# Performance work log

Measured on AMD Instinct MI355X. Metric: run time of the kernel, lower is better.

## Reference

```python
import jax, jax.numpy as jnp
import numpy as np

B, P, D, H, A, C = 256, 512, 16, 256, 8, 2
HID = 256
IN_MLP = H + A + 1  # 265


def setup_inputs() -> dict:
    key = jax.random.key(0)
    ks = jax.random.split(key, 12)
    s = 0.05  # small init for recurrent stability
    return {
        "particles": jax.random.normal(ks[0], (B, P, D), jnp.float32),
        "weights": jax.random.uniform(ks[1], (B, P), jnp.float32),
        "actions": jax.random.normal(ks[2], (B, A), jnp.float32),
        "time": jax.random.uniform(ks[3], (B,), jnp.float32) * 100.0,
        "Wi": jax.random.normal(ks[4], (D + 1, 3 * H), jnp.float32) * s,
        "bi": jnp.zeros((3 * H,), jnp.float32),
        "Wh_rz": jax.random.normal(ks[5], (H, 2 * H), jnp.float32) * s,
        "Wh_n": jax.random.normal(ks[6], (H, H), jnp.float32) * s,
        "bn": jnp.zeros((H,), jnp.float32),
        "mlp_W1": jax.random.normal(ks[7], (C, IN_MLP, HID), jnp.float32) * s,
        "mlp_b1": jnp.zeros((C, HID), jnp.float32),
        "mlp_W2": jax.random.normal(ks[8], (C, HID, HID), jnp.float32) * s,
        "mlp_b2": jnp.zeros((C, HID), jnp.float32),
        "mlp_W3": jax.random.normal(ks[9], (C, HID, 1), jnp.float32) * s,
        "mlp_b3": jnp.zeros((C, 1), jnp.float32),
        "num_time_steps": 100,
    }


def reference(particles, weights, actions, time, Wi, bi, Wh_rz, Wh_n, bn,
              mlp_W1, mlp_b1, mlp_W2, mlp_b2, mlp_W3, mlp_b3, num_time_steps):
    # feature_fn = identity; append weights as an extra feature channel
    x = jnp.concatenate([particles, weights[..., None]], axis=-1)  # [B, P, D+1]
    xs = jnp.swapaxes(x, 0, 1)  # [P, B, D+1], scan over particle axis

    def gru_step(h, xt):
        gi = xt @ Wi + bi  # [B, 3H]
        i_r, i_z, i_n = jnp.split(gi, 3, axis=-1)
        hrz = h @ Wh_rz  # [B, 2H], no bias (flax GRUCell hidden r/z dense)
        r = jax.nn.sigmoid(i_r + hrz[:, :H])
        z = jax.nn.sigmoid(i_z + hrz[:, H:])
        n = jnp.tanh(i_n + r * (h @ Wh_n + bn))
        h_new = (1.0 - z) * n + z * h
        return h_new, None

    h0 = jnp.zeros((particles.shape[0], H), particles.dtype)
    enc, _ = jax.lax.scan(gru_step, h0, xs)  # last hidden == take(outputs, -1, axis=-2)

    norm_time = time / num_time_steps
    hidden = jnp.concatenate([enc, actions, norm_time[..., None]], axis=-1)  # [B, IN_MLP]

    # n_critics MLPs evaluated batched over critic axis c
    h1 = jax.nn.relu(jnp.einsum('bi,cio->bco', hidden, mlp_W1) + mlp_b1)
    h2 = jax.nn.relu(jnp.einsum('bci,cio->bco', h1, mlp_W2) + mlp_b2)
    q = jnp.einsum('bci,cio->bco', h2, mlp_W3) + mlp_b3  # [B, C, 1]
    return q[..., 0]  # [B, C]
```

## Files before the change

### kernel.cpp

```cpp
#include <hip/hip_runtime.h>
#include <hip/hip_fp16.h>

typedef _Float16 h2v __attribute__((ext_vector_type(2)));
typedef unsigned int u32;
typedef unsigned short u16;

#define NB 256
#define NP 512
#define NH 256
#define NCOL 768

#define OFF_WH 0
#define LEN_WH 98304
#define OFF_WI (OFF_WH + LEN_WH)
#define LEN_WI 6912
#define OFF_W1 (OFF_WI + LEN_WI)
#define LEN_W1 68096
#define OFF_W2 (OFF_W1 + LEN_W1)
#define LEN_W2 65536
#define OFF_W3 (OFF_W2 + LEN_W2)
#define LEN_W3 256
#define WS_DWORDS (OFF_W3 + LEN_W3)

__device__ __forceinline__ u32 pack2(float lo, float hi) {
    h2v v; v.x = (_Float16)lo; v.y = (_Float16)hi;
    return __builtin_bit_cast(u32, v);
}

__device__ __forceinline__ float fdot2(u32 a, u32 b, float c) {
#if __has_builtin(__builtin_amdgcn_fdot2)
    return __builtin_amdgcn_fdot2(__builtin_bit_cast(h2v, a),
                                  __builtin_bit_cast(h2v, b), c, false);
#else
    h2v x = __builtin_bit_cast(h2v, a), y = __builtin_bit_cast(h2v, b);
    return c + (float)x.x * (float)y.x + (float)x.y * (float)y.y;
#endif
}

__global__ __launch_bounds__(256) void pack_kernel(
    const float* __restrict__ Wi, const float* __restrict__ Whrz,
    const float* __restrict__ Whn, const float* __restrict__ W1,
    const float* __restrict__ W2, const float* __restrict__ W3,
    u32* __restrict__ ws)
{
    for (int F = blockIdx.x * 256 + threadIdx.x; F < WS_DWORDS; F += gridDim.x * 256) {
        u32 val;
        if (F < OFF_WI) {
            int l = F & 63; int t = F >> 6;
            int i = t % 192; int wid = t / 192;
            int c = i >> 5, kk = i & 31;
            int kw = wid & 3, cg = wid >> 2;
            int k = 64 * kw + 2 * kk;
            int col = 384 * cg + 64 * c + l;
            float lo, hi;
            if (col < 512) { lo = Whrz[k * 512 + col]; hi = Whrz[(k + 1) * 512 + col]; }
            else { lo = Whn[k * 256 + (col - 512)]; hi = Whn[(k + 1) * 256 + (col - 512)]; }
            val = pack2(lo, hi);
        } else if (F < OFF_W1) {
            int j = F - OFF_WI; int kk = j / NCOL; int col = j % NCOL;
            int k = 2 * kk;
            float lo = Wi[k * NCOL + col];
            float hi = (k + 1 < 17) ? Wi[(k + 1) * NCOL + col] : 0.f;
            val = pack2(lo, hi);
        } else if (F < OFF_W2) {
            int j = F - OFF_W1; int c = j / (133 * 256); int r = j % (133 * 256);
            int kk = r >> 8; int o = r & 255;
            int k = 2 * kk;
            float lo = W1[(c * 265 + k) * 256 + o];
            float hi = (k + 1 < 265) ? W1[(c * 265 + k + 1) * 256 + o] : 0.f;
            val = pack2(lo, hi);
        } else if (F < OFF_W3) {
            int j = F - OFF_W2; int c = j >> 15; int r = j & 32767;
            int kk = r >> 8; int o = r & 255;
            float lo = W2[(c * 256 + 2 * kk) * 256 + o];
            float hi = W2[(c * 256 + 2 * kk + 1) * 256 + o];
            val = pack2(lo, hi);
        } else {
            int j = F - OFF_W3; int c = j >> 7; int jj = j & 127;
            float lo = W3[c * 256 + 2 * jj];
            float hi = W3[c * 256 + 2 * jj + 1];
            val = pack2(lo, hi);
        }
        ws[F] = val;
    }
}

__global__ __launch_bounds__(512, 2) void qnet_kernel(
    const float* __restrict__ particles, const float* __restrict__ pweights,
    const float* __restrict__ actions, const float* __restrict__ timev,
    const float* __restrict__ bi, const float* __restrict__ bn,
    const float* __restrict__ b1, const float* __restrict__ b2,
    const float* __restrict__ b3, const int* __restrict__ nts,
    const u32* __restrict__ ws, float* __restrict__ out)
{
    __shared__ __align__(16) u32 sWi[LEN_WI];
    __shared__ __align__(16) u32 sX[NP * 9];
    __shared__ __align__(16) float sPart[4 * NCOL];
    __shared__ __align__(16) u32 sH2[NH / 2];
    __shared__ __align__(16) float sHf[NH];
    __shared__ __align__(16) float sMisc[16];

    u32* sHid = sWi;
    u16* sL1 = (u16*)sX;
    u16* sL2 = (u16*)sPart;

    const int b = blockIdx.x;
    const int tid = threadIdx.x;
    const int lane = tid & 63;
    const int wid = tid >> 6;
    const int kw = wid & 3;
    const int cg = wid >> 2;

    u32 wreg[192];
    {
        const u32* gp = ws + OFF_WH + (wid * 192) * 64 + lane;
        #pragma unroll
        for (int i = 0; i < 192; ++i) wreg[i] = gp[i * 64];
    }
    for (int j = tid; j < LEN_WI; j += 512) sWi[j] = ws[OFF_WI + j];
    {
        const float4* pr = (const float4*)(particles + (long)b * NP * 16);
        for (int j = tid; j < NP * 4; j += 512) {
            float4 v = pr[j];
            int p = j >> 2, d4 = j & 3;
            sX[p * 9 + d4 * 2]     = pack2(v.x, v.y);
            sX[p * 9 + d4 * 2 + 1] = pack2(v.z, v.w);
        }
        const float* wr = pweights + (long)b * NP;
        for (int p = tid; p < NP; p += 512) sX[p * 9 + 8] = pack2(wr[p], 0.f);
    }
    if (tid < NH / 2) sH2[tid] = 0u;
    if (tid < 8) sMisc[tid] = actions[b * 8 + tid];
    if (tid == 8) sMisc[8] = timev[b] / (float)nts[0];

    float hreg = 0.f, bir = 0.f, biz = 0.f, binn = 0.f, bnn = 0.f;
    if (tid < NH) {
        bir = bi[tid]; biz = bi[NH + tid]; binn = bi[2 * NH + tid]; bnn = bn[tid];
    }
    __syncthreads();

    const int colbase = cg * 384 + lane;
    #pragma unroll 1
    for (int p = 0; p < NP; ++p) {
        float acc[6] = {0.f, 0.f, 0.f, 0.f, 0.f, 0.f};
        const uint4* h4 = ((const uint4*)sH2) + kw * 8;
        #pragma unroll
        for (int q = 0; q < 8; ++q) {
            uint4 hv = h4[q];
            u32 hp[4] = {hv.x, hv.y, hv.z, hv.w};
            #pragma unroll
            for (int j = 0; j < 4; ++j) {
                #pragma unroll
                for (int c = 0; c < 6; ++c)
                    acc[c] = fdot2(wreg[c * 32 + q * 4 + j], hp[j], acc[c]);
            }
        }
        #pragma unroll
        for (int c = 0; c < 6; ++c)
            sPart[kw * NCOL + colbase + 64 * c] = acc[c];

        float xr = 0.f, xz = 0.f, xn = 0.f;
        if (tid < NH) {
            xr = bir; xz = biz; xn = binn;
            const u32* xp = &sX[p * 9];
            #pragma unroll
            for (int kk = 0; kk < 9; ++kk) {
                u32 xv = xp[kk];
                xr = fdot2(sWi[kk * NCOL + tid], xv, xr);
                xz = fdot2(sWi[kk * NCOL + NH + tid], xv, xz);
                xn = fdot2(sWi[kk * NCOL + 2 * NH + tid], xv, xn);
            }
        }
        __syncthreads();
        if (tid < NH) {
            float sr = sPart[tid] + sPart[NCOL + tid] + sPart[2 * NCOL + tid] + sPart[3 * NCOL + tid];
            float sz = sPart[NH + tid] + sPart[NCOL + NH + tid] + sPart[2 * NCOL + NH + tid] + sPart[3 * NCOL + NH + tid];
            float sn = sPart[2 * NH + tid] + sPart[NCOL + 2 * NH + tid] + sPart[2 * NCOL + 2 * NH + tid] + sPart[3 * NCOL + 2 * NH + tid];
            float r = 1.f / (1.f + __expf(-(sr + xr)));
            float z = 1.f / (1.f + __expf(-(sz + xz)));
            float targ = xn + r * (sn + bnn);
            float e2 = __expf(2.f * targ);
            float n = 1.f - 2.f / (e2 + 1.f);
            hreg = (1.f - z) * n + z * hreg;
            _Float16 hh = (_Float16)hreg;
            ((u16*)sH2)[tid] = __builtin_bit_cast(u16, hh);
        }
        __syncthreads();
    }

    if (tid < NH) sHf[tid] = hreg;
    __syncthreads();
    if (tid < 128) sHid[tid] = pack2(sHf[2 * tid], sHf[2 * tid + 1]);
    else if (tid < 132) { int i = tid - 128; sHid[tid] = pack2(sMisc[2 * i], sMisc[2 * i + 1]); }
    else if (tid == 132) sHid[132] = pack2(sMisc[8], 0.f);
    __syncthreads();
    {
        int c = tid >> 8, o = tid & 255;
        float acc = b1[c * 256 + o];
        const u32* wp = ws + OFF_W1 + c * 133 * 256 + o;
        #pragma unroll 4
        for (int kk = 0; kk < 133; ++kk) acc = fdot2(wp[kk * 256], sHid[kk], acc);
        acc = fmaxf(acc, 0.f);
        _Float16 a16 = (_Float16)acc;
        sL1[tid] = __builtin_bit_cast(u16, a16);
    }
    __syncthreads();
    {
        int c = tid >> 8, o = tid & 255;
        float acc = b2[c * 256 + o];
        const u32* wp = ws + OFF_W2 + c * 128 * 256 + o;
        const u32* hp = (const u32*)sL1 + c * 128;
        #pragma unroll 4
        for (int kk = 0; kk < 128; ++kk) acc = fdot2(wp[kk * 256], hp[kk], acc);
        acc = fmaxf(acc, 0.f);
        _Float16 a16 = (_Float16)acc;
        sL2[tid] = __builtin_bit_cast(u16, a16);
    }
    __syncthreads();
    if (tid < 128) {
        int c = tid >> 6, l = tid & 63;
        const u32* wp = ws + OFF_W3 + c * 128;
        const u32* hp = (const u32*)sL2 + c * 128;
        float acc = fdot2(wp[l], hp[l], 0.f);
        acc = fdot2(wp[64 + l], hp[64 + l], acc);
        #pragma unroll
        for (int off = 32; off > 0; off >>= 1) acc += __shfl_down(acc, off);
        if (l == 0) out[b * 2 + c] = acc + b3[c];
    }
}

extern "C" void kernel_launch(void* const* d_in, const int* in_sizes, int n_in,
                              void* d_out, int out_size, void* d_ws, size_t ws_size,
                              hipStream_t stream) {
    const float* particles = (const float*)d_in[0];
    const float* pweights  = (const float*)d_in[1];
    const float* actions   = (const float*)d_in[2];
    const float* timev     = (const float*)d_in[3];
    const float* Wi        = (const float*)d_in[4];
    const float* bi        = (const float*)d_in[5];
    const float* Whrz      = (const float*)d_in[6];
    const float* Whn       = (const float*)d_in[7];
    const float* bn        = (const float*)d_in[8];
    const float* W1        = (const float*)d_in[9];
    const float* b1        = (const float*)d_in[10];
    const float* W2        = (const float*)d_in[11];
    const float* b2        = (const float*)d_in[12];
    const float* W3        = (const float*)d_in[13];
    const float* b3        = (const float*)d_in[14];
    const int*   nts       = (const int*)d_in[15];
    u32* ws = (u32*)d_ws;
    float* outp = (float*)d_out;

    pack_kernel<<<WS_DWORDS / 256, 256, 0, stream>>>(Wi, Whrz, Whn, W1, W2, W3, ws);
    qnet_kernel<<<NB, 512, 0, stream>>>(particles, pweights, actions, timev,
                                        bi, bn, b1, b2, b3, nts, ws, outp);
}
```

Measured before the change: 696.9 us.

## Compute GRU recurrent matvec with MFMA 16x16x32 f16 instead of fdot2

Replaces the per-step hidden-state matvec (fdot2 over register-resident weights, split across 4 k-slices with a shared-memory reduction) with MFMA 16x16x32 f16 instructions. Each wave now owns 96 full output columns over the whole K dimension. The weights are repacked as B fragments, and h is broadcast as the A operand, so only row 0 of the result is used. This removes the 4-way partial-sum reduction and cuts instruction count, at the cost of wasting 15 of the 16 MFMA rows and adding MFMA latency on the serial recurrence.

```diff
diff --git a/kernel.cpp b/kernel.cpp
--- a/kernel.cpp
+++ b/kernel.cpp
@@ -2,6 +2,8 @@
 #include <hip/hip_fp16.h>
 
 typedef _Float16 h2v __attribute__((ext_vector_type(2)));
+typedef _Float16 f16x8 __attribute__((ext_vector_type(8)));
+typedef float f32x4 __attribute__((ext_vector_type(4)));
 typedef unsigned int u32;
 typedef unsigned short u16;
 
@@ -46,12 +48,12 @@
     for (int F = blockIdx.x * 256 + threadIdx.x; F < WS_DWORDS; F += gridDim.x * 256) {
         u32 val;
         if (F < OFF_WI) {
-            int l = F & 63; int t = F >> 6;
-            int i = t % 192; int wid = t / 192;
-            int c = i >> 5, kk = i & 31;
-            int kw = wid & 3, cg = wid >> 2;
-            int k = 64 * kw + 2 * kk;
-            int col = 384 * cg + 64 * c + l;
+            int d = F & 3; int r = F >> 2;
+            int l = r & 63; int q = r >> 6;
+            int f = q % 48; int w = q / 48;
+            int t = f >> 3; int kt = f & 7;
+            int k = kt * 32 + ((l >> 4) << 3) + 2 * d;
+            int col = w * 96 + t * 16 + (l & 15);
             float lo, hi;
             if (col < 512) { lo = Whrz[k * 512 + col]; hi = Whrz[(k + 1) * 512 + col]; }
             else { lo = Whn[k * 256 + (col - 512)]; hi = Whn[(k + 1) * 256 + (col - 512)]; }
@@ -95,27 +97,25 @@
 {
     __shared__ __align__(16) u32 sWi[LEN_WI];
     __shared__ __align__(16) u32 sX[NP * 9];
-    __shared__ __align__(16) float sPart[4 * NCOL];
+    __shared__ __align__(16) float sCols[NCOL];
     __shared__ __align__(16) u32 sH2[NH / 2];
     __shared__ __align__(16) float sHf[NH];
     __shared__ __align__(16) float sMisc[16];
 
     u32* sHid = sWi;
     u16* sL1 = (u16*)sX;
-    u16* sL2 = (u16*)sPart;
+    u16* sL2 = (u16*)sCols;
 
     const int b = blockIdx.x;
     const int tid = threadIdx.x;
     const int lane = tid & 63;
     const int wid = tid >> 6;
-    const int kw = wid & 3;
-    const int cg = wid >> 2;
-
-    u32 wreg[192];
-    {
-        const u32* gp = ws + OFF_WH + (wid * 192) * 64 + lane;
+
+    f16x8 bf[48];
+    {
+        const uint4* gp = (const uint4*)(ws + OFF_WH) + (wid * 48) * 64 + lane;
         #pragma unroll
-        for (int i = 0; i < 192; ++i) wreg[i] = gp[i * 64];
+        for (int i = 0; i < 48; ++i) bf[i] = __builtin_bit_cast(f16x8, gp[i * 64]);
     }
     for (int j = tid; j < LEN_WI; j += 512) sWi[j] = ws[OFF_WI + j];
     {
@@ -139,25 +139,22 @@
     }
     __syncthreads();
 
-    const int colbase = cg * 384 + lane;
+    const uint4* h4 = ((const uint4*)sH2) + (lane >> 4);
+    float* colp = sCols + wid * 96 + (lane & 15);
+
     #pragma unroll 1
     for (int p = 0; p < NP; ++p) {
-        float acc[6] = {0.f, 0.f, 0.f, 0.f, 0.f, 0.f};
-        const uint4* h4 = ((const uint4*)sH2) + kw * 8;
+        f32x4 a0 = {0.f, 0.f, 0.f, 0.f}, a1 = a0, a2 = a0, a3 = a0, a4 = a0, a5 = a0;
         #pragma unroll
-        for (int q = 0; q < 8; ++q) {
-            uint4 hv = h4[q];
-            u32 hp[4] = {hv.x, hv.y, hv.z, hv.w};
-            #pragma unroll
-            for (int j = 0; j < 4; ++j) {
-                #pragma unroll
-                for (int c = 0; c < 6; ++c)
-                    acc[c] = fdot2(wreg[c * 32 + q * 4 + j], hp[j], acc[c]);
-            }
-        }
-        #pragma unroll
-        for (int c = 0; c < 6; ++c)
-            sPart[kw * NCOL + colbase + 64 * c] = acc[c];
+        for (int kt = 0; kt < 8; ++kt) {
+            f16x8 av = __builtin_bit_cast(f16x8, h4[kt * 4]);
+            a0 = __builtin_amdgcn_mfma_f32_16x16x32_f16(av, bf[kt],      a0, 0, 0, 0);
+            a1 = __builtin_amdgcn_mfma_f32_16x16x32_f16(av, bf[8 + kt],  a1, 0, 0, 0);
+            a2 = __builtin_amdgcn_mfma_f32_16x16x32_f16(av, bf[16 + kt], a2, 0, 0, 0);
+            a3 = __builtin_amdgcn_mfma_f32_16x16x32_f16(av, bf[24 + kt], a3, 0, 0, 0);
+            a4 = __builtin_amdgcn_mfma_f32_16x16x32_f16(av, bf[32 + kt], a4, 0, 0, 0);
+            a5 = __builtin_amdgcn_mfma_f32_16x16x32_f16(av, bf[40 + kt], a5, 0, 0, 0);
+        }
 
         float xr = 0.f, xz = 0.f, xn = 0.f;
         if (tid < NH) {
@@ -171,11 +168,16 @@
                 xn = fdot2(sWi[kk * NCOL + 2 * NH + tid], xv, xn);
             }
         }
+
+        if (lane < 16) {
+            colp[0]  = a0[0]; colp[16] = a1[0]; colp[32] = a2[0];
+            colp[48] = a3[0]; colp[64] = a4[0]; colp[80] = a5[0];
+        }
         __syncthreads();
         if (tid < NH) {
-            float sr = sPart[tid] + sPart[NCOL + tid] + sPart[2 * NCOL + tid] + sPart[3 * NCOL + tid];
-            float sz = sPart[NH + tid] + sPart[NCOL + NH + tid] + sPart[2 * NCOL + NH + tid] + sPart[3 * NCOL + NH + tid];
-            float sn = sPart[2 * NH + tid] + sPart[NCOL + 2 * NH + tid] + sPart[2 * NCOL + 2 * NH + tid] + sPart[3 * NCOL + 2 * NH + tid];
+            float sr = sCols[tid];
+            float sz = sCols[NH + tid];
+            float sn = sCols[2 * NH + tid];
             float r = 1.f / (1.f + __expf(-(sr + xr)));
             float z = 1.f / (1.f + __expf(-(sz + xz)));
             float targ = xn + r * (sn + bnn);
```

Measured after the change: 697.2 us. Within noise of the previous version (+0.0%).
